# Kernel tuning notes

Measured on AMD Instinct MI355X. Metric: run time of the kernel, lower is better.

Reference implementation:

```python
import jax, jax.numpy as jnp
import numpy as np

N = 10000      # nodes
E = 160000     # edges
D_IN = 512
D_H = 512
P_DROP = 0.2


def _glorot(key, shape):
    lim = float(np.sqrt(6.0 / (shape[0] + shape[1])))
    return jax.random.uniform(key, shape, jnp.float32, -lim, lim)


def setup_inputs() -> dict:
    key = jax.random.key(0)
    ks = jax.random.split(key, 8)
    h = jax.random.normal(ks[0], (N, D_IN), jnp.float32)
    src = jax.random.randint(ks[1], (E,), 0, N)
    dst = jax.random.randint(ks[2], (E,), 0, N)
    edge_weight = jax.random.uniform(ks[3], (E,), jnp.float32)
    W0 = _glorot(ks[4], (D_IN, D_H))
    W1 = _glorot(ks[5], (D_H, D_H))
    W2 = _glorot(ks[6], (D_H, D_H))
    b0 = jnp.zeros((D_H,), jnp.float32)
    b1 = jnp.zeros((D_H,), jnp.float32)
    b2 = jnp.zeros((D_H,), jnp.float32)
    return dict(h=h, src=src, dst=dst, edge_weight=edge_weight,
                W0=W0, b0=b0, W1=W1, b1=b1, W2=W2, b2=b2)


def _dropout(x, key):
    keep = jax.random.bernoulli(key, 1.0 - P_DROP, x.shape)
    return jnp.where(keep, x / (1.0 - P_DROP), 0.0)


def _graph_conv(x, src, dst, ew, W, b, act):
    # DGL GraphConv, norm='both', weight=True, bias=True, with edge_weight.
    ones = jnp.ones((src.shape[0],), x.dtype)
    deg_out = jnp.maximum(jax.ops.segment_sum(ones, src, num_segments=N), 1.0)
    deg_in = jnp.maximum(jax.ops.segment_sum(ones, dst, num_segments=N), 1.0)
    x = x * (deg_out ** -0.5)[:, None]          # src norm
    msg = x[src] * ew[:, None]                  # [E, D] gather + edge weight
    agg = jax.ops.segment_sum(msg, dst, num_segments=N)  # scatter-add
    out = (agg @ W) * (deg_in ** -0.5)[:, None] + b
    return act(out) if act is not None else out


def reference(h, src, dst, edge_weight, W0, b0, W1, b1, W2, b2):
    dk = jax.random.split(jax.random.key(42), 3)
    x = _dropout(h, dk[0])
    x = _graph_conv(x, src, dst, edge_weight, W0, b0, jax.nn.elu)
    x = _dropout(x, dk[1])
    x = _graph_conv(x, src, dst, edge_weight, W1, b1, jax.nn.elu)
    x = _dropout(x, dk[2])
    x = _graph_conv(x, src, dst, edge_weight, W2, b2, None)
    return x
```

## Files before the change

### kernel.cpp

```cpp
#include <hip/hip_runtime.h>
#include <stdint.h>

#define N_NODES 10000
#define N_EDGES 160000
#define D 512
#define TOT (N_NODES * D)
#define M_PAD 10112
#define NMASK (TOT / 32)

typedef _Float16 h8 __attribute__((ext_vector_type(8)));
typedef _Float16 h2 __attribute__((ext_vector_type(2)));
typedef float f4 __attribute__((ext_vector_type(4)));

__host__ __device__ inline uint32_t rotl32(uint32_t v, int r) {
    return (v << r) | (v >> (32 - r));
}

__host__ __device__ inline void tf2x32(uint32_t k0, uint32_t k1,
                                       uint32_t& x0, uint32_t& x1) {
    uint32_t k2 = k0 ^ k1 ^ 0x1BD11BDAu;
    x0 += k0; x1 += k1;
    x0 += x1; x1 = rotl32(x1, 13); x1 ^= x0;
    x0 += x1; x1 = rotl32(x1, 15); x1 ^= x0;
    x0 += x1; x1 = rotl32(x1, 26); x1 ^= x0;
    x0 += x1; x1 = rotl32(x1,  6); x1 ^= x0;
    x0 += k1; x1 += k2 + 1u;
    x0 += x1; x1 = rotl32(x1, 17); x1 ^= x0;
    x0 += x1; x1 = rotl32(x1, 29); x1 ^= x0;
    x0 += x1; x1 = rotl32(x1, 16); x1 ^= x0;
    x0 += x1; x1 = rotl32(x1, 24); x1 ^= x0;
    x0 += k2; x1 += k0 + 2u;
    x0 += x1; x1 = rotl32(x1, 13); x1 ^= x0;
    x0 += x1; x1 = rotl32(x1, 15); x1 ^= x0;
    x0 += x1; x1 = rotl32(x1, 26); x1 ^= x0;
    x0 += x1; x1 = rotl32(x1,  6); x1 ^= x0;
    x0 += k0; x1 += k1 + 3u;
    x0 += x1; x1 = rotl32(x1, 17); x1 ^= x0;
    x0 += x1; x1 = rotl32(x1, 29); x1 ^= x0;
    x0 += x1; x1 = rotl32(x1, 16); x1 ^= x0;
    x0 += x1; x1 = rotl32(x1, 24); x1 ^= x0;
    x0 += k1; x1 += k2 + 4u;
    x0 += x1; x1 = rotl32(x1, 13); x1 ^= x0;
    x0 += x1; x1 = rotl32(x1, 15); x1 ^= x0;
    x0 += x1; x1 = rotl32(x1, 26); x1 ^= x0;
    x0 += x1; x1 = rotl32(x1,  6); x1 ^= x0;
    x0 += k2; x1 += k0 + 5u;
}

__device__ __forceinline__ uint32_t dropout_bit(uint32_t k0, uint32_t k1, uint32_t j) {
    uint32_t c0 = 0u, c1 = j;
    tf2x32(k0, k1, c0, c1);
    uint32_t bits = c0 ^ c1;
    float u = __uint_as_float((bits >> 9) | 0x3f800000u) - 1.0f;
    return (u < 0.8f) ? 1u : 0u;
}

#define HIST_BLKS 625
#define WCONV_BLKS 192
#define PRE_BLKS (HIST_BLKS + WCONV_BLKS + 5000)
__global__ __launch_bounds__(256)
void pre_kernel(const int* __restrict__ src, const int* __restrict__ dst,
                int* __restrict__ deg_out, int* __restrict__ deg_in,
                const float* __restrict__ W0, const float* __restrict__ W1,
                const float* __restrict__ W2, _Float16* __restrict__ Wt,
                const float* __restrict__ x, _Float16* __restrict__ y,
                uint32_t k0, uint32_t k1) {
    __shared__ float tile[64][65];
    int b = blockIdx.x;
    int t = threadIdx.x;
    if (b < HIST_BLKS) {
        int e = b * 256 + t;
        if (e < N_EDGES) {
            atomicAdd(&deg_out[src[e]], 1);
            atomicAdd(&deg_in[dst[e]], 1);
        }
    } else if (b < HIST_BLKS + WCONV_BLKS) {
        int b2 = b - HIST_BLKS;
        int bx = b2 & 7, by = (b2 >> 3) & 7, bz = b2 >> 6;
        const float* W = (bz == 0) ? W0 : (bz == 1) ? W1 : W2;
        _Float16* T = Wt + (size_t)bz * 512 * 512;
        int r0 = by * 64, c0 = bx * 64;
        int c = t & 63, rq = t >> 6;
#pragma unroll
        for (int i = 0; i < 16; ++i) {
            int r = rq + i * 4;
            tile[r][c] = W[(size_t)(r0 + r) * 512 + c0 + c];
        }
        __syncthreads();
        int k = t & 63, nq = t >> 6;
#pragma unroll
        for (int i = 0; i < 16; ++i) {
            int n = nq + i * 4;
            T[(size_t)(c0 + n) * 512 + r0 + k] = (_Float16)tile[k][n];
        }
    } else {
        int b3 = b - HIST_BLKS - WCONV_BLKS;
        int j = (b3 * 256 + t) * 4;
        if (j >= TOT) return;
        float4 xv = *(const float4*)&x[j];
        _Float16 r[4];
        uint32_t jj = (uint32_t)j;
#pragma unroll
        for (int i = 0; i < 4; ++i) {
            float g = dropout_bit(k0, k1, jj + (uint32_t)i) ? 1.0f : 0.0f;
            float xi = (&xv.x)[i];
            r[i] = (_Float16)(g * (xi / 0.8f));
        }
        *(ushort4*)&y[j] = *(ushort4*)r;
    }
}

__global__ __launch_bounds__(1024)
void scan_kernel(const int* __restrict__ deg_in, const int* __restrict__ deg_out,
                 int* __restrict__ row_ptr,
                 float* __restrict__ rn_in, float* __restrict__ rn_out) {
    __shared__ int wsum[16];
    int tid = threadIdx.x;
    int lane = tid & 63, wv = tid >> 6;
    int base = tid * 10;
    int v[10];
    int tot = 0;
#pragma unroll
    for (int i = 0; i < 10; ++i) {
        int idx = base + i;
        v[i] = (idx < N_NODES) ? deg_in[idx] : 0;
        tot += v[i];
    }
    int s = tot;
#pragma unroll
    for (int off = 1; off < 64; off <<= 1) {
        int t = __shfl_up(s, off, 64);
        if (lane >= off) s += t;
    }
    if (lane == 63) wsum[wv] = s;
    __syncthreads();
    if (wv == 0 && lane < 16) {
        int ws = wsum[lane];
#pragma unroll
        for (int off = 1; off < 16; off <<= 1) {
            int t = __shfl_up(ws, off, 64);
            if (lane >= off) ws += t;
        }
        wsum[lane] = ws;
    }
    __syncthreads();
    int run = ((wv > 0) ? wsum[wv - 1] : 0) + (s - tot);
#pragma unroll
    for (int i = 0; i < 10; ++i) {
        int idx = base + i;
        if (idx < N_NODES) {
            row_ptr[idx] = run;
            rn_in[idx]  = 1.0f / sqrtf(fmaxf((float)v[i], 1.0f));
            rn_out[idx] = 1.0f / sqrtf(fmaxf((float)deg_out[idx], 1.0f));
        }
        run += v[i];
    }
    if (tid == 1023) row_ptr[N_NODES] = wsum[15];
}

__global__ void fill_kernel(const int* __restrict__ src, const int* __restrict__ dst,
                            const float* __restrict__ ew, const int* __restrict__ row_ptr,
                            const float* __restrict__ rn_out,
                            int* __restrict__ cursor, int2* __restrict__ csr) {
    int e = blockIdx.x * 256 + threadIdx.x;
    if (e >= N_EDGES) return;
    int v = dst[e];
    int sn = src[e];
    int pos = atomicAdd(&cursor[v], 1);
    int idx = row_ptr[v] + pos;
    csr[idx] = make_int2(sn, __float_as_int(ew[e] * rn_out[sn]));
}

__global__ __launch_bounds__(256)
void aggregate_kernel(const _Float16* __restrict__ y, const int* __restrict__ row_ptr,
                      const int2* __restrict__ csr, _Float16* __restrict__ agg,
                      uint32_t* __restrict__ mask, uint32_t mk0, uint32_t mk1) {
    int node = blockIdx.x * 4 + (threadIdx.x >> 6);
    int lane = threadIdx.x & 63;
    int cs = blockIdx.y;
    const _Float16* ys = y + cs * 128 + lane * 2;
    int beg = row_ptr[node], end = row_ptr[node + 1];
    float a0 = 0.f, a1 = 0.f;
    int k = beg;
    for (; k + 7 < end; k += 8) {
        int2 e[8];
#pragma unroll
        for (int i = 0; i < 8; ++i) e[i] = csr[k + i];
        h2 v[8];
#pragma unroll
        for (int i = 0; i < 8; ++i) v[i] = *(const h2*)&ys[(size_t)e[i].x * 512];
#pragma unroll
        for (int i = 0; i < 8; ++i) {
            float w = __int_as_float(e[i].y);
            a0 += w * (float)v[i][0];
            a1 += w * (float)v[i][1];
        }
    }
    for (; k < end; ++k) {
        int2 e0 = csr[k];
        float w = __int_as_float(e0.y);
        h2 v = *(const h2*)&ys[(size_t)e0.x * 512];
        a0 += w * (float)v[0];
        a1 += w * (float)v[1];
    }
    h2 r;
    r[0] = (_Float16)a0;
    r[1] = (_Float16)a1;
    *(h2*)&agg[(size_t)node * 512 + cs * 128 + lane * 2] = r;

    if (cs == 0 && mask) {
        int gtid = blockIdx.x * 256 + threadIdx.x;
        if (gtid < NMASK) {
            uint32_t w = 0, jb = (uint32_t)gtid * 32u;
#pragma unroll 4
            for (int i = 0; i < 32; ++i)
                w |= dropout_bit(mk0, mk1, jb + (uint32_t)i) << i;
            mask[gtid] = w;
        }
    }
}

#define GBK 128
#define LDA2 136
__global__ __launch_bounds__(256)
void gemm_kernel(const _Float16* __restrict__ A, const _Float16* __restrict__ Wt,
                 const float* __restrict__ bias, const float* __restrict__ rn_in,
                 _Float16* __restrict__ yout, float* __restrict__ fout,
                 int mode, const uint32_t* __restrict__ mask) {
    __shared__ _Float16 As[64 * LDA2];
    __shared__ _Float16 Bs[64 * LDA2];
    int tid = threadIdx.x;
    int wv = tid >> 6, lane = tid & 63;

    int f = blockIdx.x;
    int T = (f & 7) * 158 + (f >> 3);
    int row0 = (T >> 3) * 64, col0 = (T & 7) * 64;

    int wr = wv >> 1, wc = wv & 1;

    f4 acc[2][2];
#pragma unroll
    for (int i = 0; i < 2; ++i)
#pragma unroll
        for (int j = 0; j < 2; ++j) acc[i][j] = (f4){0.f, 0.f, 0.f, 0.f};

    int r = tid >> 2;
    int cseg = (tid & 3) * 32;
    const _Float16* gA = A  + (size_t)(row0 + r) * 512 + cseg;
    const _Float16* gB = Wt + (size_t)(col0 + r) * 512 + cseg;
    _Float16* wA = &As[r * LDA2 + cseg];
    _Float16* wB = &Bs[r * LDA2 + cseg];

    const _Float16* fa = &As[(wr * 32 + (lane & 15)) * LDA2 + (lane >> 4) * 8];
    const _Float16* fb = &Bs[(wc * 32 + (lane & 15)) * LDA2 + (lane >> 4) * 8];

    h8 ra[4], rb[4];
#pragma unroll
    for (int i = 0; i < 4; ++i) {
        ra[i] = *(const h8*)(gA + i * 8);
        rb[i] = *(const h8*)(gB + i * 8);
    }

    for (int kk = 0; kk < 512; kk += GBK) {
#pragma unroll
        for (int i = 0; i < 4; ++i) {
            *(h8*)(wA + i * 8) = ra[i];
            *(h8*)(wB + i * 8) = rb[i];
        }
        __syncthreads();
        if (kk + GBK < 512) {
#pragma unroll
            for (int i = 0; i < 4; ++i) {
                ra[i] = *(const h8*)(gA + kk + GBK + i * 8);
                rb[i] = *(const h8*)(gB + kk + GBK + i * 8);
            }
        }
#pragma unroll
        for (int s = 0; s < 4; ++s) {
            h8 af0 = *(const h8*)(fa + s * 32);
            h8 af1 = *(const h8*)(fa + 16 * LDA2 + s * 32);
            h8 bf0 = *(const h8*)(fb + s * 32);
            h8 bf1 = *(const h8*)(fb + 16 * LDA2 + s * 32);
            acc[0][0] = __builtin_amdgcn_mfma_f32_16x16x32_f16(af0, bf0, acc[0][0], 0, 0, 0);
            acc[0][1] = __builtin_amdgcn_mfma_f32_16x16x32_f16(af0, bf1, acc[0][1], 0, 0, 0);
            acc[1][0] = __builtin_amdgcn_mfma_f32_16x16x32_f16(af1, bf0, acc[1][0], 0, 0, 0);
            acc[1][1] = __builtin_amdgcn_mfma_f32_16x16x32_f16(af1, bf1, acc[1][1], 0, 0, 0);
        }
        __syncthreads();
    }

    int mbase = row0 + wr * 32;
    int nbase = col0 + wc * 32;
#pragma unroll
    for (int mt = 0; mt < 2; ++mt) {
#pragma unroll
        for (int nt = 0; nt < 2; ++nt) {
            int gr0 = mbase + mt * 16 + (lane >> 4) * 4;
            int gc = nbase + nt * 16 + (lane & 15);
            float bcol = bias[gc];
#pragma unroll
            for (int i = 0; i < 4; ++i) {
                int gr = gr0 + i;
                if (gr >= N_NODES) continue;
                float v = acc[mt][nt][i] * rn_in[gr] + bcol;
                if (mode == 0) {
                    v = (v > 0.f) ? v : expm1f(v);
                    uint32_t j = (uint32_t)(gr * 512 + gc);
                    uint32_t g = (mask[j >> 5] >> (j & 31)) & 1u;
                    v = g ? (v / 0.8f) : 0.0f;
                    yout[(size_t)gr * 512 + gc] = (_Float16)v;
                } else {
                    fout[(size_t)gr * 512 + gc] = v;
                }
            }
        }
    }
}

extern "C" void kernel_launch(void* const* d_in, const int* in_sizes, int n_in,
                              void* d_out, int out_size, void* d_ws, size_t ws_size,
                              hipStream_t stream) {
    const float* h   = (const float*)d_in[0];
    const int*   src = (const int*)d_in[1];
    const int*   dst = (const int*)d_in[2];
    const float* ew  = (const float*)d_in[3];
    const float* W0  = (const float*)d_in[4];
    const float* b0  = (const float*)d_in[5];
    const float* W1  = (const float*)d_in[6];
    const float* b1  = (const float*)d_in[7];
    const float* W2  = (const float*)d_in[8];
    const float* b2  = (const float*)d_in[9];
    const float* bl[3] = {b0, b1, b2};
    float* out = (float*)d_out;

    char* ws = (char*)d_ws;
    _Float16* y16  = (_Float16*)ws; ws += (size_t)TOT * 2;
    _Float16* aggF = (_Float16*)ws; ws += (size_t)M_PAD * 512 * 2;
    _Float16* Wt   = (_Float16*)ws; ws += (size_t)3 * 512 * 512 * 2;
    int* degi_in  = (int*)ws;  ws += N_NODES * 4;
    int* degi_out = (int*)ws;  ws += N_NODES * 4;
    int* cursor   = (int*)ws;  ws += N_NODES * 4;
    int* row_ptr  = (int*)ws;  ws += (N_NODES + 1) * 4;
    ws = (char*)(((uintptr_t)ws + 15) & ~(uintptr_t)15);
    int2* csr     = (int2*)ws; ws += (size_t)N_EDGES * 8;
    float* rn_in  = (float*)ws; ws += N_NODES * 4;
    float* rn_out = (float*)ws; ws += N_NODES * 4;
    uint32_t* maskbuf = (uint32_t*)ws; ws += (size_t)NMASK * 4;

    hipMemsetAsync(degi_in, 0, 3 * N_NODES * 4, stream);

    uint32_t dk[3][2];
    for (int i = 0; i < 3; ++i) {
        uint32_t c0 = 0u, c1 = (uint32_t)i;
        tf2x32(0u, 42u, c0, c1);
        dk[i][0] = c0; dk[i][1] = c1;
    }

    pre_kernel<<<PRE_BLKS, 256, 0, stream>>>(src, dst, degi_out, degi_in,
                                             W0, W1, W2, Wt, h, y16,
                                             dk[0][0], dk[0][1]);
    scan_kernel<<<1, 1024, 0, stream>>>(degi_in, degi_out, row_ptr, rn_in, rn_out);
    fill_kernel<<<(N_EDGES + 255) / 256, 256, 0, stream>>>(src, dst, ew, row_ptr,
                                                           rn_out, cursor, csr);

    for (int l = 0; l < 3; ++l) {
        uint32_t* mk = (l < 2) ? maskbuf : nullptr;
        uint32_t mk0 = (l < 2) ? dk[l + 1][0] : 0u;
        uint32_t mk1 = (l < 2) ? dk[l + 1][1] : 0u;
        aggregate_kernel<<<dim3(N_NODES / 4, 4), 256, 0, stream>>>(
            y16, row_ptr, csr, aggF, mk, mk0, mk1);
        int mode = (l < 2) ? 0 : 1;
        gemm_kernel<<<1264, 256, 0, stream>>>(
            aggF, Wt + (size_t)l * 512 * 512, bl[l], rn_in,
            y16, out, mode, maskbuf);
    }
}
```

Before: 329.5 us.

## Widen aggregate gathers to full-row h8 loads and split mask generation into blocks

The aggregate kernel now has each wavefront process a whole 512-wide node row, with every lane loading 8 halves (16 bytes) per edge. Previously there were four column-slice blocks with 4-byte loads. This cuts redundant CSR reads and raises memory-transaction width. Dropout mask generation moves to its own trailing blocks instead of piggybacking on the cs==0 slice. It also swaps division by 0.8 for multiplication by 1.25 and expm1f for __expf-1, which may change ELU rounding slightly for small negative inputs.

```diff
diff --git a/kernel.cpp b/kernel.cpp
--- a/kernel.cpp
+++ b/kernel.cpp
@@ -7,9 +7,10 @@
 #define TOT (N_NODES * D)
 #define M_PAD 10112
 #define NMASK (TOT / 32)
+#define AGG_BLKS 2500
+#define MASK_BLKS 625
 
 typedef _Float16 h8 __attribute__((ext_vector_type(8)));
-typedef _Float16 h2 __attribute__((ext_vector_type(2)));
 typedef float f4 __attribute__((ext_vector_type(4)));
 
 __host__ __device__ inline uint32_t rotl32(uint32_t v, int r) {
@@ -104,7 +105,7 @@
         for (int i = 0; i < 4; ++i) {
             float g = dropout_bit(k0, k1, jj + (uint32_t)i) ? 1.0f : 0.0f;
             float xi = (&xv.x)[i];
-            r[i] = (_Float16)(g * (xi / 0.8f));
+            r[i] = (_Float16)(g * (xi * 1.25f));
         }
         *(ushort4*)&y[j] = *(ushort4*)r;
     }
@@ -175,41 +176,10 @@
 void aggregate_kernel(const _Float16* __restrict__ y, const int* __restrict__ row_ptr,
                       const int2* __restrict__ csr, _Float16* __restrict__ agg,
                       uint32_t* __restrict__ mask, uint32_t mk0, uint32_t mk1) {
-    int node = blockIdx.x * 4 + (threadIdx.x >> 6);
-    int lane = threadIdx.x & 63;
-    int cs = blockIdx.y;
-    const _Float16* ys = y + cs * 128 + lane * 2;
-    int beg = row_ptr[node], end = row_ptr[node + 1];
-    float a0 = 0.f, a1 = 0.f;
-    int k = beg;
-    for (; k + 7 < end; k += 8) {
-        int2 e[8];
-#pragma unroll
-        for (int i = 0; i < 8; ++i) e[i] = csr[k + i];
-        h2 v[8];
-#pragma unroll
-        for (int i = 0; i < 8; ++i) v[i] = *(const h2*)&ys[(size_t)e[i].x * 512];
-#pragma unroll
-        for (int i = 0; i < 8; ++i) {
-            float w = __int_as_float(e[i].y);
-            a0 += w * (float)v[i][0];
-            a1 += w * (float)v[i][1];
-        }
-    }
-    for (; k < end; ++k) {
-        int2 e0 = csr[k];
-        float w = __int_as_float(e0.y);
-        h2 v = *(const h2*)&ys[(size_t)e0.x * 512];
-        a0 += w * (float)v[0];
-        a1 += w * (float)v[1];
-    }
-    h2 r;
-    r[0] = (_Float16)a0;
-    r[1] = (_Float16)a1;
-    *(h2*)&agg[(size_t)node * 512 + cs * 128 + lane * 2] = r;
-
-    if (cs == 0 && mask) {
-        int gtid = blockIdx.x * 256 + threadIdx.x;
+    int b = blockIdx.x;
+    if (b >= AGG_BLKS) {
+        if (mask == nullptr) return;
+        int gtid = (b - AGG_BLKS) * 256 + threadIdx.x;
         if (gtid < NMASK) {
             uint32_t w = 0, jb = (uint32_t)gtid * 32u;
 #pragma unroll 4
@@ -217,7 +187,39 @@
                 w |= dropout_bit(mk0, mk1, jb + (uint32_t)i) << i;
             mask[gtid] = w;
         }
-    }
+        return;
+    }
+    int node = b * 4 + (threadIdx.x >> 6);
+    int lane = threadIdx.x & 63;
+    int beg = row_ptr[node], end = row_ptr[node + 1];
+    const _Float16* yl = y + lane * 8;
+    float acc[8] = {0, 0, 0, 0, 0, 0, 0, 0};
+    int k = beg;
+    for (; k + 7 < end; k += 8) {
+        int2 e[8];
+#pragma unroll
+        for (int i = 0; i < 8; ++i) e[i] = csr[k + i];
+        h8 v[8];
+#pragma unroll
+        for (int i = 0; i < 8; ++i) v[i] = *(const h8*)&yl[(size_t)e[i].x * 512];
+#pragma unroll
+        for (int i = 0; i < 8; ++i) {
+            float w = __int_as_float(e[i].y);
+#pragma unroll
+            for (int j = 0; j < 8; ++j) acc[j] += w * (float)v[i][j];
+        }
+    }
+    for (; k < end; ++k) {
+        int2 e0 = csr[k];
+        float w = __int_as_float(e0.y);
+        h8 v = *(const h8*)&yl[(size_t)e0.x * 512];
+#pragma unroll
+        for (int j = 0; j < 8; ++j) acc[j] += w * (float)v[j];
+    }
+    _Float16 r[8];
+#pragma unroll
+    for (int j = 0; j < 8; ++j) r[j] = (_Float16)acc[j];
+    *(h8*)&agg[(size_t)node * 512 + lane * 8] = *(h8*)r;
 }
 
 #define GBK 128
@@ -304,10 +306,10 @@
                 if (gr >= N_NODES) continue;
                 float v = acc[mt][nt][i] * rn_in[gr] + bcol;
                 if (mode == 0) {
-                    v = (v > 0.f) ? v : expm1f(v);
+                    v = (v > 0.f) ? v : (__expf(v) - 1.0f);
                     uint32_t j = (uint32_t)(gr * 512 + gc);
                     uint32_t g = (mask[j >> 5] >> (j & 31)) & 1u;
-                    v = g ? (v / 0.8f) : 0.0f;
+                    v = g ? (v * 1.25f) : 0.0f;
                     yout[(size_t)gr * 512 + gc] = (_Float16)v;
                 } else {
                     fout[(size_t)gr * 512 + gc] = v;
@@ -367,7 +369,7 @@
         uint32_t* mk = (l < 2) ? maskbuf : nullptr;
         uint32_t mk0 = (l < 2) ? dk[l + 1][0] : 0u;
         uint32_t mk1 = (l < 2) ? dk[l + 1][1] : 0u;
-        aggregate_kernel<<<dim3(N_NODES / 4, 4), 256, 0, stream>>>(
+        aggregate_kernel<<<AGG_BLKS + MASK_BLKS, 256, 0, stream>>>(
             y16, row_ptr, csr, aggF, mk, mk0, mk1);
         int mode = (l < 2) ? 0 : 1;
         gemm_kernel<<<1264, 256, 0, stream>>>(
```

New measurement: 316.3 us. -4.0%, faster.
